# Kernel optimization log

Hardware: AMD Instinct MI355X
Metric: run time of the kernel (lower is better)

## Reference

```python
import jax, jax.numpy as jnp
import numpy as np

B, D_IN, LAT, C = 16384, 512, 64, 8
HID = [1024, 512, 256]

def _lin(k, fi, fo, scale=0.02):
    k1, k2 = jax.random.split(k)
    return jax.random.normal(k1, (fi, fo), jnp.float32) * scale, jax.random.normal(k2, (fo,), jnp.float32) * scale

def _lin_c(k, fi, fo, scale=0.02):
    k1, k2 = jax.random.split(k)
    return jax.random.normal(k1, (C, fi, fo), jnp.float32) * scale, jax.random.normal(k2, (C, fo), jnp.float32) * scale

def setup_inputs() -> dict:
    key = jax.random.key(0)
    ks = jax.random.split(key, 16)
    x = jax.random.normal(ks[0], (B, D_IN), jnp.float32)
    cluster_labels = jax.random.randint(ks[1], (B,), 0, C, jnp.int32)
    eps = jax.random.normal(ks[2], (B, LAT), jnp.float32)
    # encoder: shared(512->1024), unshared(1024->512), shared(512->256)
    enc_W0, enc_b0 = _lin(ks[3], D_IN, HID[0])
    enc_Wu, enc_bu = _lin_c(ks[4], HID[0], HID[1])
    enc_W2, enc_b2 = _lin(ks[5], HID[1], HID[2])
    # shared latent heads
    mu_W, mu_b = _lin(ks[6], HID[2], LAT)
    lv_W, lv_b = _lin(ks[7], HID[2], LAT)
    # decoder (hidden_dims reversed = [256,512,1024]): unshared(64->256), shared(256->512), unshared(512->1024)
    dec_Wu0, dec_bu0 = _lin_c(ks[8], LAT, HID[2])
    dec_W1, dec_b1 = _lin(ks[9], HID[2], HID[1])
    dec_Wu2, dec_bu2 = _lin_c(ks[10], HID[1], HID[0])
    # per-cluster final layer (1024 -> input_dim), no activation (all-continuous)
    fin_W, fin_b = _lin_c(ks[11], HID[0], D_IN)
    return dict(x=x, cluster_labels=cluster_labels, eps=eps,
                enc_W0=enc_W0, enc_b0=enc_b0, enc_Wu=enc_Wu, enc_bu=enc_bu,
                enc_W2=enc_W2, enc_b2=enc_b2, mu_W=mu_W, mu_b=mu_b,
                lv_W=lv_W, lv_b=lv_b, dec_Wu0=dec_Wu0, dec_bu0=dec_bu0,
                dec_W1=dec_W1, dec_b1=dec_b1, dec_Wu2=dec_Wu2, dec_bu2=dec_bu2,
                fin_W=fin_W, fin_b=fin_b)

def _unshared(h, W, b, labels):
    # per-cluster GEMM then row-wise combine (mask-based dispatch, no row reorder)
    y = jnp.einsum('bi,cio->bco', h, W) + b[None]  # [B, C, out]
    return jnp.take_along_axis(y, labels[:, None, None], axis=1)[:, 0, :]

def reference(x, cluster_labels, eps,
              enc_W0, enc_b0, enc_Wu, enc_bu, enc_W2, enc_b2,
              mu_W, mu_b, lv_W, lv_b,
              dec_Wu0, dec_bu0, dec_W1, dec_b1, dec_Wu2, dec_bu2,
              fin_W, fin_b):
    lbl = cluster_labels.astype(jnp.int32)
    # encoder
    h = jax.nn.relu(x @ enc_W0 + enc_b0)
    h = jax.nn.relu(_unshared(h, enc_Wu, enc_bu, lbl))
    h = jax.nn.relu(h @ enc_W2 + enc_b2)
    mu = h @ mu_W + mu_b
    logvar = h @ lv_W + lv_b
    # reparameterize
    z = mu + jnp.exp(0.5 * logvar) * eps
    # decoder
    h = jax.nn.relu(_unshared(z, dec_Wu0, dec_bu0, lbl))
    h = jax.nn.relu(h @ dec_W1 + dec_b1)
    h = jax.nn.relu(_unshared(h, dec_Wu2, dec_bu2, lbl))
    # per-cluster final output layer (identity activation: all-continuous)
    recon = _unshared(h, fin_W, fin_b, lbl)
    return recon
```

## Files before the change

### kernel.cpp

```cpp
#include <hip/hip_runtime.h>

typedef _Float16 f16;
typedef __attribute__((ext_vector_type(8))) _Float16 f16x8;
typedef __attribute__((ext_vector_type(4))) _Float16 f16x4;
typedef __attribute__((ext_vector_type(4))) float    f32x4;

#define B_ROWS 16384
#define MPAD   17408
#define MTILES 136
#define NBLK   64

typedef __attribute__((address_space(1))) void as1_void;
typedef __attribute__((address_space(3))) void as3_void;

__device__ __forceinline__ void gl_lds16(const void* g, void* l) {
    __builtin_amdgcn_global_load_lds((const as1_void*)g, (as3_void*)l, 16, 0, 0);
}


__global__ __launch_bounds__(256) void k_prep(const int* __restrict__ lbl, int* __restrict__ blockhist,
                                              int* __restrict__ rowmap,
                                              const float* __restrict__ mb_, const float* __restrict__ lb_,
                                              float* __restrict__ bz, f16* __restrict__ zerob) {
    int b = blockIdx.x, t = threadIdx.x;
    int i = b * 256 + t;
    rowmap[i] = -1;
    if (b < NBLK) {
        __shared__ int h[8];
        if (t < 8) h[t] = 0;
        __syncthreads();
        atomicAdd(&h[lbl[i]], 1);
        __syncthreads();
        if (t < 8) blockhist[b * 8 + t] = h[t];
    } else if (b == NBLK) {
        if (t < 64) zerob[t] = (f16)0.f;
        if (t < 64) bz[t] = mb_[t];
        else if (t < 128) bz[t] = lb_[t - 64];
    }
}

__global__ void k_offsets(const int* __restrict__ blockhist, int* offs, int* tilec, int* blockbase) {
    __shared__ int tot[8];
    __shared__ int so[9];
    int t = threadIdx.x;
    if (t < 8) {
        int s = 0;
        for (int b = 0; b < NBLK; ++b) s += blockhist[b * 8 + t];
        tot[t] = s;
    }
    __syncthreads();
    if (t == 0) {
        int o = 0;
        for (int c = 0; c < 8; ++c) { so[c] = o; o += (tot[c] + 127) & ~127; }
        so[8] = o;
        for (int c = 0; c < 9; ++c) offs[c] = so[c];
    }
    __syncthreads();
    if (t < 8) {
        int run = so[t];
        for (int b = 0; b < NBLK; ++b) {
            blockbase[b * 8 + t] = run;
            run += blockhist[b * 8 + t];
        }
    }
    if (t < MTILES) {
        int row = t * 128, c = 7;
        for (int cc = 0; cc < 8; ++cc)
            if (row >= so[cc] && row < so[cc + 1]) c = cc;
        tilec[t] = c;
    }
}

__global__ __launch_bounds__(256) void k_scatter(const int* __restrict__ lbl,
                                                 const int* __restrict__ blockbase,
                                                 int* __restrict__ rowmap) {
    __shared__ int cur[8];
    if (threadIdx.x < 8) cur[threadIdx.x] = blockbase[blockIdx.x * 8 + threadIdx.x];
    __syncthreads();
    int i = blockIdx.x * 256 + threadIdx.x;
    int c = lbl[i];
    int pos = atomicAdd(&cur[c], 1);
    rowmap[pos] = i;
}


struct Seg { const float* s; f16* d; int K, N, b0, nx, ny; long sCS, dCS; };
struct SegTab { Seg g[10]; };

__global__ __launch_bounds__(256) void k_trans(SegTab tab, const float* __restrict__ x, f16* __restrict__ xh) {
    int bid = blockIdx.x;
    int t = threadIdx.x;
    if (bid < tab.g[1].b0) {
        long i = (long)bid * 256 + t;
        const float4* xs = (const float4*)x;
        float4 v0 = xs[i * 2], v1 = xs[i * 2 + 1];
        f16x8 o = {(f16)v0.x, (f16)v0.y, (f16)v0.z, (f16)v0.w,
                   (f16)v1.x, (f16)v1.y, (f16)v1.z, (f16)v1.w};
        ((f16x8*)xh)[i] = o;
        return;
    }
    int s = 9;
    while (bid < tab.g[s].b0) --s;
    Seg sg = tab.g[s];
    int lb = bid - sg.b0;
    int nxy = sg.nx * sg.ny;
    int z = lb / nxy; int r = lb - z * nxy;
    int by = r / sg.nx; int bx = r - by * sg.nx;
    const float* src = sg.s + (size_t)z * sg.sCS;
    f16* dst = sg.d + (size_t)z * sg.dCS;
    int k0 = by * 64, n0 = bx * 64;

    __shared__ f16 tr[64][88];
    int a = t & 15, b = t >> 4;
    float4 v[4];
    #pragma unroll
    for (int i = 0; i < 4; ++i)
        v[i] = *(const float4*)&src[(size_t)(k0 + b * 4 + i) * sg.N + n0 + a * 4];
    #pragma unroll
    for (int j = 0; j < 4; ++j) {
        f16x4 w = {(f16)((const float*)&v[0])[j], (f16)((const float*)&v[1])[j],
                   (f16)((const float*)&v[2])[j], (f16)((const float*)&v[3])[j]};
        *(f16x4*)&tr[a * 4 + j][b * 4] = w;
    }
    __syncthreads();
    int n = t >> 2, s4 = t & 3;
    f16x8 o0 = *(const f16x8*)&tr[n][s4 * 16];
    f16x8 o1 = *(const f16x8*)&tr[n][s4 * 16 + 8];
    *(f16x8*)&dst[(size_t)(n0 + n) * sg.K + k0 + s4 * 16] = o0;
    *(f16x8*)&dst[(size_t)(n0 + n) * sg.K + k0 + s4 * 16 + 8] = o1;
}

__global__ __launch_bounds__(256) void k_reparam(const f16* __restrict__ muv, const float* __restrict__ eps,
                                                 const int* __restrict__ rowmap, f16* __restrict__ z) {
    int i = blockIdx.x * 256 + threadIdx.x;
    int p = i >> 6, j = i & 63;
    int g = rowmap[p];
    float e  = (g >= 0) ? eps[(size_t)g * 64 + j] : 0.f;
    float mu = (float)muv[(size_t)p * 128 + j];
    float lv = (float)muv[(size_t)p * 128 + 64 + j];
    z[i] = (f16)(mu + expf(0.5f * lv) * e);
}


template<int GATHER, int PERW, int RELU, int SCATTER>
__global__ __launch_bounds__(256, 2) void gemm_k(
    const f16* __restrict__ A, const f16* __restrict__ Wt,
    const float* __restrict__ bias, f16* __restrict__ Out, float* __restrict__ OutF,
    const int* __restrict__ rowmap, const int* __restrict__ tilec,
    const f16* __restrict__ zerobuf, int K, int N)
{
    __shared__ __align__(16) f16 lA[2][128 * 64];
    __shared__ __align__(16) f16 lB[2][128 * 64];
    const int tid  = threadIdx.x;
    const int wave = tid >> 6;
    const int lane = tid & 63;

    const int id  = blockIdx.x;
    const int xcd = id & 7;
    const int jj  = id >> 3;
    const int tm  = (jj % 17) * 8 + xcd;
    const int tn  = jj / 17;
    const int r0 = tm * 128, n0 = tn * 128;

    const f16* wb = Wt;
    const float* bb = bias;
    if (PERW) {
        int c = tilec[tm];
        wb += (size_t)c * K * N;
        bb += (size_t)c * N;
    }

    const int srow = tid >> 3;
    const int sg   = tid & 7;
    const int xk16 = (sg ^ (srow & 7)) * 16;
    const size_t rowB = (size_t)K * 2;
    const size_t passB = 32 * rowB;

    const char* pa[4]; size_t stepA[4];
    #pragma unroll
    for (int p = 0; p < 4; ++p) {
        int gr = r0 + p * 32 + srow;
        if (GATHER) {
            int g = rowmap[gr];
            if (g >= 0) { pa[p] = (const char*)(A + (size_t)g * K) + xk16; stepA[p] = 128; }
            else        { pa[p] = (const char*)zerobuf;                    stepA[p] = 0;   }
        } else {
            pa[p] = (const char*)(A + (size_t)gr * K) + xk16; stepA[p] = 128;
        }
    }
    const char* pb = (const char*)(wb + (size_t)(n0 + srow) * K) + xk16;

    const int mb = (wave >> 1) * 64;
    const int nb = (wave & 1) * 64;
    const int quad = lane >> 4;
    const int r16  = lane & 15;
    const int key  = r16 & 7;

    f32x4 acc[4][4];
    #pragma unroll
    for (int i = 0; i < 4; ++i)
        #pragma unroll
        for (int j = 0; j < 4; ++j)
            acc[i][j] = (f32x4){0.f, 0.f, 0.f, 0.f};

    const int nk = K >> 6;

    #pragma unroll
    for (int p = 0; p < 4; ++p)
        gl_lds16(pa[p], (char*)lA[0] + p * 4096 + wave * 1024);
    #pragma unroll
    for (int p = 0; p < 4; ++p)
        gl_lds16(pb + p * passB, (char*)lB[0] + p * 4096 + wave * 1024);
    #pragma unroll
    for (int p = 0; p < 4; ++p) pa[p] += stepA[p];
    pb += 128;

    for (int kb = 0; kb < nk; ++kb) {
        const int cur = kb & 1, nxt = cur ^ 1;
        __syncthreads();
        if (kb + 1 < nk) {
            #pragma unroll
            for (int p = 0; p < 4; ++p)
                gl_lds16(pa[p], (char*)lA[nxt] + p * 4096 + wave * 1024);
            #pragma unroll
            for (int p = 0; p < 4; ++p)
                gl_lds16(pb + p * passB, (char*)lB[nxt] + p * 4096 + wave * 1024);
            #pragma unroll
            for (int p = 0; p < 4; ++p) pa[p] += stepA[p];
            pb += 128;
        }
        #pragma unroll
        for (int kk = 0; kk < 2; ++kk) {
            const int off = ((kk * 4 + quad) ^ key) * 16;
            f16x8 af[4], bf[4];
            #pragma unroll
            for (int i = 0; i < 4; ++i)
                af[i] = *(const f16x8*)((const char*)lA[cur] + (mb + i * 16 + r16) * 128 + off);
            #pragma unroll
            for (int j = 0; j < 4; ++j)
                bf[j] = *(const f16x8*)((const char*)lB[cur] + (nb + j * 16 + r16) * 128 + off);
            #pragma unroll
            for (int i = 0; i < 4; ++i)
                #pragma unroll
                for (int j = 0; j < 4; ++j)
                    acc[i][j] = __builtin_amdgcn_mfma_f32_16x16x32_f16(af[i], bf[j], acc[i][j], 0, 0, 0);
        }
    }

    float bv[4];
    #pragma unroll
    for (int j = 0; j < 4; ++j) bv[j] = bb[n0 + nb + j * 16 + r16];

    #pragma unroll
    for (int i = 0; i < 4; ++i) {
        #pragma unroll
        for (int r = 0; r < 4; ++r) {
            int orow = r0 + mb + i * 16 + quad * 4 + r;
            int g = 0;
            if (SCATTER) g = rowmap[orow];
            #pragma unroll
            for (int j = 0; j < 4; ++j) {
                int ocol = n0 + nb + j * 16 + r16;
                float v = acc[i][j][r] + bv[j];
                if (RELU) v = fmaxf(v, 0.f);
                if (SCATTER) {
                    if (g >= 0) OutF[(size_t)g * N + ocol] = v;
                } else {
                    Out[(size_t)orow * N + ocol] = (f16)v;
                }
            }
        }
    }
}


extern "C" void kernel_launch(void* const* d_in, const int* in_sizes, int n_in,
                              void* d_out, int out_size, void* d_ws, size_t ws_size,
                              hipStream_t stream) {
    const float* x      = (const float*)d_in[0];
    const int*   lbl    = (const int*)  d_in[1];
    const float* eps    = (const float*)d_in[2];
    const float* enc_W0 = (const float*)d_in[3];
    const float* enc_b0 = (const float*)d_in[4];
    const float* enc_Wu = (const float*)d_in[5];
    const float* enc_bu = (const float*)d_in[6];
    const float* enc_W2 = (const float*)d_in[7];
    const float* enc_b2 = (const float*)d_in[8];
    const float* mu_W   = (const float*)d_in[9];
    const float* mu_b   = (const float*)d_in[10];
    const float* lv_W   = (const float*)d_in[11];
    const float* lv_b   = (const float*)d_in[12];
    const float* dWu0   = (const float*)d_in[13];
    const float* dbu0   = (const float*)d_in[14];
    const float* dW1    = (const float*)d_in[15];
    const float* db1    = (const float*)d_in[16];
    const float* dWu2   = (const float*)d_in[17];
    const float* dbu2   = (const float*)d_in[18];
    const float* finW   = (const float*)d_in[19];
    const float* finb   = (const float*)d_in[20];
    float* out = (float*)d_out;
    (void)in_sizes; (void)n_in; (void)out_size; (void)ws_size;

    char* base = (char*)d_ws;
    size_t off = 0;
    auto alloc = [&](size_t bytes) { char* r = base + off; off = (off + bytes + 255) & ~(size_t)255; return r; };
    f16* xh     = (f16*)alloc((size_t)B_ROWS * 512 * 2);
    f16* buf1   = (f16*)alloc((size_t)MPAD * 1024 * 2);
    f16* buf2   = (f16*)alloc((size_t)MPAD * 512 * 2);
    f16* buf3   = (f16*)alloc((size_t)MPAD * 256 * 2);
    f16* muv    = (f16*)alloc((size_t)MPAD * 128 * 2);
    f16* zb     = (f16*)alloc((size_t)MPAD * 64 * 2);
    f16* w0t    = (f16*)alloc(1024ul * 512 * 2);
    f16* wut    = (f16*)alloc(8ul * 512 * 1024 * 2);
    f16* w2t    = (f16*)alloc(256ul * 512 * 2);
    f16* wzt    = (f16*)alloc(128ul * 256 * 2);
    f16* wd0t   = (f16*)alloc(8ul * 256 * 64 * 2);
    f16* wd1t   = (f16*)alloc(512ul * 256 * 2);
    f16* wd2t   = (f16*)alloc(8ul * 1024 * 512 * 2);
    f16* wft    = (f16*)alloc(8ul * 512 * 1024 * 2);
    float* bz   = (float*)alloc(128 * 4);
    int* rowmap = (int*)alloc(MPAD * 4);
    int* blockhist = (int*)alloc(NBLK * 8 * 4);
    int* blockbase = (int*)alloc(NBLK * 8 * 4);
    int* offs   = (int*)alloc(64);
    int* tilec  = (int*)alloc(MTILES * 4);
    f16* zerob  = (f16*)alloc(256);

    k_prep<<<MPAD / 256, 256, 0, stream>>>(lbl, blockhist, rowmap, mu_b, lv_b, bz, zerob);
    k_offsets<<<1, 256, 0, stream>>>(blockhist, offs, tilec, blockbase);
    k_scatter<<<NBLK, 256, 0, stream>>>(lbl, blockbase, rowmap);

    SegTab tab;
    int b0 = B_ROWS * 512 / 8 / 256;
    auto seg = [&](int i, const float* s, f16* d, int K, int N, int nz, long sCS, long dCS) {
        int nx = N / 64, ny = K / 64;
        tab.g[i] = Seg{s, d, K, N, b0, nx, ny, sCS, dCS};
        b0 += nx * ny * nz;
    };
    tab.g[0] = Seg{nullptr, nullptr, 0, 0, 0, 0, 0, 0, 0};
    seg(1, enc_W0, w0t, 512, 1024, 1, 0, 0);
    seg(2, enc_Wu, wut, 1024, 512, 8, 1024l * 512, 512l * 1024);
    seg(3, enc_W2, w2t, 512, 256, 1, 0, 0);
    seg(4, mu_W, wzt, 256, 64, 1, 0, 0);
    seg(5, lv_W, wzt + 64 * 256, 256, 64, 1, 0, 0);
    seg(6, dWu0, wd0t, 64, 256, 8, 64l * 256, 256l * 64);
    seg(7, dW1, wd1t, 256, 512, 1, 0, 0);
    seg(8, dWu2, wd2t, 512, 1024, 8, 512l * 1024, 1024l * 512);
    seg(9, finW, wft, 1024, 512, 8, 1024l * 512, 512l * 1024);
    k_trans<<<b0, 256, 0, stream>>>(tab, x, xh);

    gemm_k<1,0,1,0><<<MTILES * 8, 256, 0, stream>>>(xh,   w0t,  enc_b0, buf1, nullptr, rowmap, tilec, zerob, 512, 1024);
    gemm_k<0,1,1,0><<<MTILES * 4, 256, 0, stream>>>(buf1, wut,  enc_bu, buf2, nullptr, rowmap, tilec, zerob, 1024, 512);
    gemm_k<0,0,1,0><<<MTILES * 2, 256, 0, stream>>>(buf2, w2t,  enc_b2, buf3, nullptr, rowmap, tilec, zerob, 512, 256);
    gemm_k<0,0,0,0><<<MTILES * 1, 256, 0, stream>>>(buf3, wzt,  bz,     muv,  nullptr, rowmap, tilec, zerob, 256, 128);
    k_reparam<<<MPAD * 64 / 256, 256, 0, stream>>>(muv, eps, rowmap, zb);
    gemm_k<0,1,1,0><<<MTILES * 2, 256, 0, stream>>>(zb,   wd0t, dbu0,   buf3, nullptr, rowmap, tilec, zerob, 64, 256);
    gemm_k<0,0,1,0><<<MTILES * 4, 256, 0, stream>>>(buf3, wd1t, db1,    buf2, nullptr, rowmap, tilec, zerob, 256, 512);
    gemm_k<0,1,1,0><<<MTILES * 8, 256, 0, stream>>>(buf2, wd2t, dbu2,   buf1, nullptr, rowmap, tilec, zerob, 512, 1024);
    gemm_k<0,1,0,1><<<MTILES * 4, 256, 0, stream>>>(buf1, wft,  finb,   nullptr, out,  rowmap, tilec, zerob, 1024, 512);
}
```

Before: 374.7 us.

## Add 256x256-tile GEMM kernel and pad cluster segments to 256 rows

```diff
diff --git a/kernel.cpp b/kernel.cpp
--- a/kernel.cpp
+++ b/kernel.cpp
@@ -6,8 +6,9 @@
 typedef __attribute__((ext_vector_type(4))) float    f32x4;
 
 #define B_ROWS 16384
-#define MPAD   17408
-#define MTILES 136
+#define MPAD   18432
+#define MT256  72
+#define MT128  144
 #define NBLK   64
 
 typedef __attribute__((address_space(1))) void as1_void;
@@ -39,7 +40,8 @@
     }
 }
 
-__global__ void k_offsets(const int* __restrict__ blockhist, int* offs, int* tilec, int* blockbase) {
+__global__ void k_offsets(const int* __restrict__ blockhist, int* offs, int* tilec256, int* tilec128,
+                          int* blockbase) {
     __shared__ int tot[8];
     __shared__ int so[9];
     int t = threadIdx.x;
@@ -51,7 +53,7 @@
     __syncthreads();
     if (t == 0) {
         int o = 0;
-        for (int c = 0; c < 8; ++c) { so[c] = o; o += (tot[c] + 127) & ~127; }
+        for (int c = 0; c < 8; ++c) { so[c] = o; o += (tot[c] + 255) & ~255; }
         so[8] = o;
         for (int c = 0; c < 9; ++c) offs[c] = so[c];
     }
@@ -63,11 +65,17 @@
             run += blockhist[b * 8 + t];
         }
     }
-    if (t < MTILES) {
+    if (t < MT256) {
+        int row = t * 256, c = 7;
+        for (int cc = 0; cc < 8; ++cc)
+            if (row >= so[cc] && row < so[cc + 1]) c = cc;
+        tilec256[t] = c;
+    }
+    if (t < MT128) {
         int row = t * 128, c = 7;
         for (int cc = 0; cc < 8; ++cc)
             if (row >= so[cc] && row < so[cc + 1]) c = cc;
-        tilec[t] = c;
+        tilec128[t] = c;
     }
 }
 
@@ -139,6 +147,129 @@
     float mu = (float)muv[(size_t)p * 128 + j];
     float lv = (float)muv[(size_t)p * 128 + 64 + j];
     z[i] = (f16)(mu + expf(0.5f * lv) * e);
+}
+
+
+template<int GATHER, int PERW, int RELU, int SCATTER>
+__global__ __launch_bounds__(512, 2) void gemm2(
+    const f16* __restrict__ A, const f16* __restrict__ Wt,
+    const float* __restrict__ bias, f16* __restrict__ Out, float* __restrict__ OutF,
+    const int* __restrict__ rowmap, const int* __restrict__ tilec,
+    const f16* __restrict__ zerobuf, int K, int N)
+{
+    __shared__ __align__(16) f16 lA[2][256 * 32];
+    __shared__ __align__(16) f16 lB[2][256 * 32];
+    const int tid  = threadIdx.x;
+    const int wave = tid >> 6;
+    const int lane = tid & 63;
+
+    const int id  = blockIdx.x;
+    const int xcd = id & 7;
+    const int jj  = id >> 3;
+    const int tm  = (jj % 9) * 8 + xcd;
+    const int tn  = jj / 9;
+    const int r0 = tm * 256, n0 = tn * 256;
+
+    const f16* wb = Wt;
+    const float* bb = bias;
+    if (PERW) {
+        int c = tilec[tm];
+        wb += (size_t)c * K * N;
+        bb += (size_t)c * N;
+    }
+
+    const int srow = tid >> 2;
+    const int sg   = tid & 3;
+    const int xk16 = (sg ^ (srow & 3)) * 16;
+
+    const char* pa[2]; size_t stepA[2];
+    #pragma unroll
+    for (int p = 0; p < 2; ++p) {
+        int gr = r0 + p * 128 + srow;
+        if (GATHER) {
+            int g = rowmap[gr];
+            if (g >= 0) { pa[p] = (const char*)(A + (size_t)g * K) + xk16; stepA[p] = 64; }
+            else        { pa[p] = (const char*)zerobuf;                    stepA[p] = 0;  }
+        } else {
+            pa[p] = (const char*)(A + (size_t)gr * K) + xk16; stepA[p] = 64;
+        }
+    }
+    const char* pb[2];
+    #pragma unroll
+    for (int p = 0; p < 2; ++p)
+        pb[p] = (const char*)(wb + (size_t)(n0 + p * 128 + srow) * K) + xk16;
+
+    const int wm = wave & 3, wn = wave >> 2;
+    const int mb = wm * 64, nb = wn * 128;
+    const int quad = lane >> 4;
+    const int r16  = lane & 15;
+    const int key  = r16 & 3;
+
+    f32x4 acc[4][8];
+    #pragma unroll
+    for (int i = 0; i < 4; ++i)
+        #pragma unroll
+        for (int j = 0; j < 8; ++j)
+            acc[i][j] = (f32x4){0.f, 0.f, 0.f, 0.f};
+
+    const int nk = K >> 5;
+
+    #pragma unroll
+    for (int p = 0; p < 2; ++p) {
+        gl_lds16(pa[p], (char*)lA[0] + p * 8192 + wave * 1024);
+        gl_lds16(pb[p], (char*)lB[0] + p * 8192 + wave * 1024);
+        pa[p] += stepA[p]; pb[p] += 64;
+    }
+
+    for (int kb = 0; kb < nk; ++kb) {
+        const int cur = kb & 1, nxt = cur ^ 1;
+        __syncthreads();
+        if (kb + 1 < nk) {
+            #pragma unroll
+            for (int p = 0; p < 2; ++p) {
+                gl_lds16(pa[p], (char*)lA[nxt] + p * 8192 + wave * 1024);
+                gl_lds16(pb[p], (char*)lB[nxt] + p * 8192 + wave * 1024);
+                pa[p] += stepA[p]; pb[p] += 64;
+            }
+        }
+        f16x8 af[4], bf[8];
+        #pragma unroll
+        for (int i = 0; i < 4; ++i)
+            af[i] = *(const f16x8*)((const char*)lA[cur] + (mb + i * 16 + r16) * 64 + ((quad ^ key) * 16));
+        #pragma unroll
+        for (int j = 0; j < 8; ++j)
+            bf[j] = *(const f16x8*)((const char*)lB[cur] + (nb + j * 16 + r16) * 64 + ((quad ^ key) * 16));
+        #pragma unroll
+        for (int i = 0; i < 4; ++i)
+            #pragma unroll
+            for (int j = 0; j < 8; ++j)
+                acc[i][j] = __builtin_amdgcn_mfma_f32_16x16x32_f16(af[i], bf[j], acc[i][j], 0, 0, 0);
+    }
+
+    float bv[8];
+    #pragma unroll
+    for (int j = 0; j < 8; ++j) bv[j] = bb[n0 + nb + j * 16 + r16];
+
+    #pragma unroll
+    for (int i = 0; i < 4; ++i) {
+        #pragma unroll
+        for (int r = 0; r < 4; ++r) {
+            int orow = r0 + mb + i * 16 + quad * 4 + r;
+            int g = 0;
+            if (SCATTER) g = rowmap[orow];
+            #pragma unroll
+            for (int j = 0; j < 8; ++j) {
+                int ocol = n0 + nb + j * 16 + r16;
+                float v = acc[i][j][r] + bv[j];
+                if (RELU) v = fmaxf(v, 0.f);
+                if (SCATTER) {
+                    if (g >= 0) OutF[(size_t)g * N + ocol] = v;
+                } else {
+                    Out[(size_t)orow * N + ocol] = (f16)v;
+                }
+            }
+        }
+    }
 }
 
 
@@ -158,8 +289,8 @@
     const int id  = blockIdx.x;
     const int xcd = id & 7;
     const int jj  = id >> 3;
-    const int tm  = (jj % 17) * 8 + xcd;
-    const int tn  = jj / 17;
+    const int tm  = (jj % 18) * 8 + xcd;
+    const int tn  = jj / 18;
     const int r0 = tm * 128, n0 = tn * 128;
 
     const f16* wb = Wt;
@@ -323,11 +454,12 @@
     int* blockhist = (int*)alloc(NBLK * 8 * 4);
     int* blockbase = (int*)alloc(NBLK * 8 * 4);
     int* offs   = (int*)alloc(64);
-    int* tilec  = (int*)alloc(MTILES * 4);
+    int* tilec256 = (int*)alloc(MT256 * 4);
+    int* tilec128 = (int*)alloc(MT128 * 4);
     f16* zerob  = (f16*)alloc(256);
 
     k_prep<<<MPAD / 256, 256, 0, stream>>>(lbl, blockhist, rowmap, mu_b, lv_b, bz, zerob);
-    k_offsets<<<1, 256, 0, stream>>>(blockhist, offs, tilec, blockbase);
+    k_offsets<<<1, 256, 0, stream>>>(blockhist, offs, tilec256, tilec128, blockbase);
     k_scatter<<<NBLK, 256, 0, stream>>>(lbl, blockbase, rowmap);
 
     SegTab tab;
@@ -349,13 +481,13 @@
     seg(9, finW, wft, 1024, 512, 8, 1024l * 512, 512l * 1024);
     k_trans<<<b0, 256, 0, stream>>>(tab, x, xh);
 
-    gemm_k<1,0,1,0><<<MTILES * 8, 256, 0, stream>>>(xh,   w0t,  enc_b0, buf1, nullptr, rowmap, tilec, zerob, 512, 1024);
-    gemm_k<0,1,1,0><<<MTILES * 4, 256, 0, stream>>>(buf1, wut,  enc_bu, buf2, nullptr, rowmap, tilec, zerob, 1024, 512);
-    gemm_k<0,0,1,0><<<MTILES * 2, 256, 0, stream>>>(buf2, w2t,  enc_b2, buf3, nullptr, rowmap, tilec, zerob, 512, 256);
-    gemm_k<0,0,0,0><<<MTILES * 1, 256, 0, stream>>>(buf3, wzt,  bz,     muv,  nullptr, rowmap, tilec, zerob, 256, 128);
+    gemm2<1,0,1,0><<<MT256 * 4, 512, 0, stream>>>(xh,   w0t,  enc_b0, buf1, nullptr, rowmap, tilec256, zerob, 512, 1024);
+    gemm2<0,1,1,0><<<MT256 * 2, 512, 0, stream>>>(buf1, wut,  enc_bu, buf2, nullptr, rowmap, tilec256, zerob, 1024, 512);
+    gemm2<0,0,1,0><<<MT256 * 1, 512, 0, stream>>>(buf2, w2t,  enc_b2, buf3, nullptr, rowmap, tilec256, zerob, 512, 256);
+    gemm_k<0,0,0,0><<<MT128 * 1, 256, 0, stream>>>(buf3, wzt,  bz,     muv,  nullptr, rowmap, tilec128, zerob, 256, 128);
     k_reparam<<<MPAD * 64 / 256, 256, 0, stream>>>(muv, eps, rowmap, zb);
-    gemm_k<0,1,1,0><<<MTILES * 2, 256, 0, stream>>>(zb,   wd0t, dbu0,   buf3, nullptr, rowmap, tilec, zerob, 64, 256);
-    gemm_k<0,0,1,0><<<MTILES * 4, 256, 0, stream>>>(buf3, wd1t, db1,    buf2, nullptr, rowmap, tilec, zerob, 256, 512);
-    gemm_k<0,1,1,0><<<MTILES * 8, 256, 0, stream>>>(buf2, wd2t, dbu2,   buf1, nullptr, rowmap, tilec, zerob, 512, 1024);
-    gemm_k<0,1,0,1><<<MTILES * 4, 256, 0, stream>>>(buf1, wft,  finb,   nullptr, out,  rowmap, tilec, zerob, 1024, 512);
-}
+    gemm_k<0,1,1,0><<<MT128 * 2, 256, 0, stream>>>(zb,   wd0t, dbu0,   buf3, nullptr, rowmap, tilec128, zerob, 64, 256);
+    gemm2<0,0,1,0><<<MT256 * 2, 512, 0, stream>>>(buf3, wd1t, db1,    buf2, nullptr, rowmap, tilec256, zerob, 256, 512);
+    gemm2<0,1,1,0><<<MT256 * 4, 512, 0, stream>>>(buf2, wd2t, dbu2,   buf1, nullptr, rowmap, tilec256, zerob, 512, 1024);
+    gemm2<0,1,0,1><<<MT256 * 2, 512, 0, stream>>>(buf1, wft,  finb,   nullptr, out,  rowmap, tilec256, zerob, 1024, 512);
+}
```

Measured after the change: 425.1 us. +13.5%, slower.
